# Optimization experiments

Measured on AMD Instinct MI355X. Metric: run time of the kernel, lower is better.

Reference implementation:

```python
import jax, jax.numpy as jnp
import numpy as np

EPS = 1e-4

def _mp_normalize(x):
    # EDM2-style normalize: divide by (eps + RMS-scaled L2 norm) along last dim -> unit RMS
    n = jnp.linalg.norm(x, axis=-1, keepdims=True)
    n = EPS + n * (1.0 / np.sqrt(x.shape[-1]))
    return x / n

def _mp_linear(x, w):
    # magnitude-preserving linear: row-normalized weight scaled by 1/sqrt(fan_in), no bias
    fan_in = w.shape[-1]
    w_hat = _mp_normalize(w) * (1.0 / np.sqrt(fan_in))
    return x @ w_hat.T

def setup_inputs() -> dict:
    key = jax.random.key(0)
    k1, k2, k3 = jax.random.split(key, 3)
    B, T, D = 2, 2048, 1024
    x = jax.random.normal(k1, (B, T, D), dtype=jnp.float32)
    w_qkv = jax.random.normal(k2, (3 * D, D), dtype=jnp.float32)
    w_out = jax.random.normal(k3, (D, D), dtype=jnp.float32)
    return {"x": x, "w_qkv": w_qkv, "w_out": w_out}

def reference(x, w_qkv, w_out):
    B, T, D = x.shape
    H = 16
    hd = D // H
    scale = 1.0 / np.sqrt(hd)

    qkv = _mp_linear(x, w_qkv)                      # (B, T, 3D)
    q, k, v = jnp.split(qkv, 3, axis=-1)            # each (B, T, D)

    def to_heads(t):
        return t.reshape(B, T, H, hd).transpose(0, 2, 1, 3)  # (B, H, T, hd)

    q, k, v = to_heads(q), to_heads(k), to_heads(v)
    q = _mp_normalize(q)
    k = _mp_normalize(k)

    scores = jnp.einsum("bhqd,bhkd->bhqk", q, k) * scale
    attn = jax.nn.softmax(scores, axis=-1)
    out = jnp.einsum("bhqk,bhkd->bhqd", attn, v)    # (B, H, T, hd)
    out = out.transpose(0, 2, 1, 3).reshape(B, T, D)
    return _mp_linear(out, w_out)
```

## Files before the change

kernel.cpp:

```cpp
#include <hip/hip_runtime.h>

#define BATCH  2
#define SEQ    2048
#define DMODEL 1024
#define NHEAD  16
#define HDIM   64
#define NROWS  (BATCH * SEQ)
#define QKVC   (3 * DMODEL)

typedef float f32x4 __attribute__((ext_vector_type(4)));
typedef float f32x16 __attribute__((ext_vector_type(16)));
typedef short s16x8 __attribute__((ext_vector_type(8)));
typedef short s16x4 __attribute__((ext_vector_type(4)));
typedef unsigned int u32x4 __attribute__((ext_vector_type(4)));

__device__ __forceinline__ unsigned short f2bf(float f) {
  unsigned int u = __float_as_uint(f);
  u = (u + 0x7FFFu + ((u >> 16) & 1u)) >> 16;
  return (unsigned short)u;
}
__device__ __forceinline__ float bf2f(unsigned short s) {
  return __uint_as_float(((unsigned int)s) << 16);
}
__device__ __forceinline__ unsigned pkbf(float a, float b) {
  unsigned r;
  asm("v_cvt_pk_bf16_f32 %0, %1, %2" : "=v"(r) : "v"(a), "v"(b));
  return r;
}
__device__ __forceinline__ void swp(unsigned &a, unsigned &b) {
  asm volatile("v_permlane32_swap_b32 %0, %1" : "+v"(a), "+v"(b));
}

__global__ __launch_bounds__(256) void k_wnorm(const float* __restrict__ Wq_src,
                                               const float* __restrict__ Wo_src,
                                               unsigned short* __restrict__ Wq,
                                               unsigned short* __restrict__ Wo) {
  const int row = blockIdx.x, tid = threadIdx.x;
  const float* src = (row < QKVC) ? (Wq_src + (size_t)row * DMODEL)
                                  : (Wo_src + (size_t)(row - QKVC) * DMODEL);
  unsigned short* dst = (row < QKVC) ? (Wq + (size_t)row * DMODEL)
                                     : (Wo + (size_t)(row - QKVC) * DMODEL);
  float4 v = ((const float4*)src)[tid];
  float ss = v.x * v.x + v.y * v.y + v.z * v.z + v.w * v.w;
#pragma unroll
  for (int m = 1; m < 64; m <<= 1) ss += __shfl_xor(ss, m);
  __shared__ float part[4];
  if ((tid & 63) == 0) part[tid >> 6] = ss;
  __syncthreads();
  const float tot = part[0] + part[1] + part[2] + part[3];
  const float scale = 0.03125f / (1e-4f + sqrtf(tot) * 0.03125f);
  unsigned short* op = dst + tid * 4;
  op[0] = f2bf(v.x * scale); op[1] = f2bf(v.y * scale);
  op[2] = f2bf(v.z * scale); op[3] = f2bf(v.w * scale);
}

__global__ __launch_bounds__(256) void k_cast(const float* __restrict__ X,
                                              unsigned short* __restrict__ Xb) {
  const int i = blockIdx.x * 256 + threadIdx.x;
  const float4 v = ((const float4*)X)[i];
  ushort4 o = { f2bf(v.x), f2bf(v.y), f2bf(v.z), f2bf(v.w) };
  ((ushort4*)Xb)[i] = o;
}

#define LDP 88
template <int WRITE_BF16>
__global__ __launch_bounds__(256, 3) void k_gemm_bt(const unsigned short* __restrict__ A,
                                                    const unsigned short* __restrict__ Bm,
                                                    void* __restrict__ Cv,
                                                    int M, int N, int K) {
  __shared__ unsigned short As[128 * LDP];
  __shared__ unsigned short Bs[128 * LDP];
  const int tid = threadIdx.x;
  const int nbn = N >> 7;
  const int bm = (blockIdx.x / nbn) << 7;
  const int bn = (blockIdx.x % nbn) << 7;
  const int wave = tid >> 6, lane = tid & 63;
  const int wr = (wave >> 1) << 6, wc = (wave & 1) << 6;
  const int l16 = lane & 15, lg = lane >> 4;

  f32x4 acc[4][4];
#pragma unroll
  for (int m = 0; m < 4; ++m)
#pragma unroll
    for (int n = 0; n < 4; ++n) acc[m][n] = (f32x4){0.f, 0.f, 0.f, 0.f};

  s16x8 ra[4], rb[4];
#pragma unroll
  for (int it = 0; it < 4; ++it) {
    const int c = it * 256 + tid;
    const int r = c >> 3, col = (c & 7) << 3;
    ra[it] = *(const s16x8*)(A + (size_t)(bm + r) * K + col);
    rb[it] = *(const s16x8*)(Bm + (size_t)(bn + r) * K + col);
  }

  for (int k0 = 0; k0 < K; k0 += 64) {
    __syncthreads();
#pragma unroll
    for (int it = 0; it < 4; ++it) {
      const int c = it * 256 + tid;
      const int r = c >> 3, col = (c & 7) << 3;
      *(s16x8*)(As + r * LDP + col) = ra[it];
      *(s16x8*)(Bs + r * LDP + col) = rb[it];
    }
    __syncthreads();
    if (k0 + 64 < K) {
#pragma unroll
      for (int it = 0; it < 4; ++it) {
        const int c = it * 256 + tid;
        const int r = c >> 3, col = (c & 7) << 3;
        ra[it] = *(const s16x8*)(A + (size_t)(bm + r) * K + k0 + 64 + col);
        rb[it] = *(const s16x8*)(Bm + (size_t)(bn + r) * K + k0 + 64 + col);
      }
    }
#pragma unroll
    for (int ks = 0; ks < 2; ++ks) {
      s16x8 af[4], bq[4];
#pragma unroll
      for (int m = 0; m < 4; ++m)
        af[m] = *(const s16x8*)(As + (wr + m * 16 + l16) * LDP + ks * 32 + lg * 8);
#pragma unroll
      for (int n = 0; n < 4; ++n)
        bq[n] = *(const s16x8*)(Bs + (wc + n * 16 + l16) * LDP + ks * 32 + lg * 8);
#pragma unroll
      for (int m = 0; m < 4; ++m)
#pragma unroll
        for (int n = 0; n < 4; ++n)
          acc[m][n] = __builtin_amdgcn_mfma_f32_16x16x32_bf16(af[m], bq[n], acc[m][n], 0, 0, 0);
    }
  }
  if (WRITE_BF16) {
    unsigned short* C = (unsigned short*)Cv;
#pragma unroll
    for (int m = 0; m < 4; ++m)
#pragma unroll
      for (int n = 0; n < 4; ++n)
#pragma unroll
        for (int r = 0; r < 4; ++r)
          C[(size_t)(bm + wr + m * 16 + lg * 4 + r) * N + (bn + wc + n * 16 + l16)] =
              f2bf(acc[m][n][r]);
  } else {
    float* C = (float*)Cv;
#pragma unroll
    for (int m = 0; m < 4; ++m)
#pragma unroll
      for (int n = 0; n < 4; ++n)
#pragma unroll
        for (int r = 0; r < 4; ++r)
          C[(size_t)(bm + wr + m * 16 + lg * 4 + r) * N + (bn + wc + n * 16 + l16)] =
              acc[m][n][r];
  }
}

__global__ __launch_bounds__(256) void k_qknorm(unsigned short* __restrict__ qkv) {
  const int row = blockIdx.x, tid = threadIdx.x;
  const int hv = tid >> 3, g = tid & 7;
  const int base = (hv < 16) ? (hv * HDIM) : (DMODEL + (hv - 16) * HDIM);
  unsigned short* p = qkv + (size_t)row * QKVC + base + g * 8;
  s16x8 v = *(const s16x8*)p;
  float f[8];
  float ss = 0.f;
#pragma unroll
  for (int j = 0; j < 8; ++j) { f[j] = bf2f((unsigned short)v[j]); ss += f[j] * f[j]; }
  ss += __shfl_xor(ss, 1); ss += __shfl_xor(ss, 2); ss += __shfl_xor(ss, 4);
  float scale = 1.f / (1e-4f + sqrtf(ss) * 0.125f);
  if (hv < 16) scale *= 0.125f;
  s16x8 o;
#pragma unroll
  for (int j = 0; j < 8; ++j) o[j] = (short)f2bf(f[j] * scale);
  *(s16x8*)p = o;
}

__global__ __launch_bounds__(256) void k_vtrans(const unsigned short* __restrict__ qkv,
                                                unsigned short* __restrict__ Vt) {
  const int tt = blockIdx.x & 31, bh = blockIdx.x >> 5;
  const int b = bh >> 4, h = bh & 15;
  const int t0 = tt * 64;
  __shared__ unsigned short tile[64][80];
  const int tid = threadIdx.x;
#pragma unroll
  for (int half = 0; half < 2; ++half) {
    const int tl = half * 32 + (tid >> 3), part = tid & 7;
    s16x8 v = *(const s16x8*)(qkv + (size_t)(b * SEQ + t0 + tl) * QKVC + 2 * DMODEL +
                              h * HDIM + part * 8);
    *(s16x8*)(&tile[tl][part * 8]) = v;
  }
  __syncthreads();
#pragma unroll
  for (int half = 0; half < 2; ++half) {
    const int d = half * 32 + (tid >> 3), tp = tid & 7;
    s16x8 o;
#pragma unroll
    for (int j = 0; j < 8; ++j) o[j] = (short)tile[tp * 8 + j][d];
    *(s16x8*)(Vt + (size_t)(bh * HDIM + d) * SEQ + t0 + tp * 8) = o;
  }
}

__global__ __launch_bounds__(256) void k_attn(const unsigned short* __restrict__ qkv,
                                              const unsigned short* __restrict__ Vt,
                                              unsigned short* __restrict__ O) {
  const int bid = blockIdx.x;
  const int logical = ((bid & 7) << 6) + (bid >> 3);
  const int bh = logical >> 4, qt = logical & 15;
  const int b = bh >> 4, h = bh & 15;
  const int tid = threadIdx.x;
  const int wave = tid >> 6, lane = tid & 63;
  const int l31 = lane & 31, hi = lane >> 5;
  const int q0 = qt * 128 + wave * 32;

  __shared__ s16x8 ks[64 * 8];
  __shared__ s16x8 vs[64 * 8];

  const unsigned short* qp =
      qkv + (size_t)(b * SEQ + q0 + l31) * QKVC + h * HDIM + hi * 8;
  const s16x8 qf0 = *(const s16x8*)(qp);
  const s16x8 qf1 = *(const s16x8*)(qp + 16);
  const s16x8 qf2 = *(const s16x8*)(qp + 32);
  const s16x8 qf3 = *(const s16x8*)(qp + 48);

  const int srow = tid >> 3, chunk = tid & 7;
  const unsigned short* ksrc =
      qkv + (size_t)(b * SEQ + srow) * QKVC + DMODEL + h * HDIM + chunk * 8;
  const unsigned short* vsrc =
      Vt + (size_t)(bh * HDIM + srow) * SEQ + chunk * 8;
  const int wsl = srow * 8 + (chunk ^ (srow & 7));
  const int wsh = wsl + 32 * 8;

  f32x16 acc0 = {0,0,0,0,0,0,0,0,0,0,0,0,0,0,0,0};
  f32x16 acc1 = {0,0,0,0,0,0,0,0,0,0,0,0,0,0,0,0};
  float l = 0.f;

  s16x8 rk0 = *(const s16x8*)(ksrc);
  s16x8 rk1 = *(const s16x8*)(ksrc + (size_t)32 * QKVC);
  s16x8 rv0 = *(const s16x8*)(vsrc);
  s16x8 rv1 = *(const s16x8*)(vsrc + (size_t)32 * SEQ);

  for (int kt = 0; kt < SEQ; kt += 64) {
    __syncthreads();
    ks[wsl] = rk0; ks[wsh] = rk1;
    vs[wsl] = rv0; vs[wsh] = rv1;
    __syncthreads();
    if (kt + 64 < SEQ) {
      rk0 = *(const s16x8*)(ksrc + (size_t)(kt + 64) * QKVC);
      rk1 = *(const s16x8*)(ksrc + (size_t)(kt + 96) * QKVC);
      rv0 = *(const s16x8*)(vsrc + kt + 64);
      rv1 = *(const s16x8*)(vsrc + (size_t)32 * SEQ + kt + 64);
    }
#pragma unroll
    for (int kh = 0; kh < 2; ++kh) {
      const int key = kh * 32 + l31;
      const int kb = key * 8, kx = key & 7;
      f32x16 st = {0,0,0,0,0,0,0,0,0,0,0,0,0,0,0,0};
      st = __builtin_amdgcn_mfma_f32_32x32x16_bf16(ks[kb + ((0 + hi) ^ kx)], qf0, st, 0, 0, 0);
      st = __builtin_amdgcn_mfma_f32_32x32x16_bf16(ks[kb + ((2 + hi) ^ kx)], qf1, st, 0, 0, 0);
      st = __builtin_amdgcn_mfma_f32_32x32x16_bf16(ks[kb + ((4 + hi) ^ kx)], qf2, st, 0, 0, 0);
      st = __builtin_amdgcn_mfma_f32_32x32x16_bf16(ks[kb + ((6 + hi) ^ kx)], qf3, st, 0, 0, 0);

#pragma unroll
      for (int r = 0; r < 16; ++r) st[r] = __expf(st[r] - 8.f);

      float s0 = (st[0] + st[1]) + (st[2] + st[3]);
      float s1 = (st[4] + st[5]) + (st[6] + st[7]);
      float s2 = (st[8] + st[9]) + (st[10] + st[11]);
      float s3 = (st[12] + st[13]) + (st[14] + st[15]);
      l += (s0 + s1) + (s2 + s3);

      unsigned P0 = pkbf(st[0], st[1]),   P1 = pkbf(st[2], st[3]);
      unsigned P2 = pkbf(st[4], st[5]),   P3 = pkbf(st[6], st[7]);
      unsigned P4 = pkbf(st[8], st[9]),   P5 = pkbf(st[10], st[11]);
      unsigned P6 = pkbf(st[12], st[13]), P7 = pkbf(st[14], st[15]);
      swp(P0, P2);
      swp(P1, P3);
      swp(P4, P6);
      swp(P5, P7);
      u32x4 w0; w0[0] = P0; w0[1] = P1; w0[2] = P2; w0[3] = P3;
      u32x4 w1; w1[0] = P4; w1[1] = P5; w1[2] = P6; w1[3] = P7;
      const s16x8 pf0 = __builtin_bit_cast(s16x8, w0);
      const s16x8 pf1 = __builtin_bit_cast(s16x8, w1);

      const int vb0 = l31 * 8,        vx0 = l31 & 7;
      const int vb1 = (l31 + 32) * 8, vx1 = vx0;
      acc0 = __builtin_amdgcn_mfma_f32_32x32x16_bf16(vs[vb0 + ((kh * 4 + 0 + hi) ^ vx0)], pf0, acc0, 0, 0, 0);
      acc0 = __builtin_amdgcn_mfma_f32_32x32x16_bf16(vs[vb0 + ((kh * 4 + 2 + hi) ^ vx0)], pf1, acc0, 0, 0, 0);
      acc1 = __builtin_amdgcn_mfma_f32_32x32x16_bf16(vs[vb1 + ((kh * 4 + 0 + hi) ^ vx1)], pf0, acc1, 0, 0, 0);
      acc1 = __builtin_amdgcn_mfma_f32_32x32x16_bf16(vs[vb1 + ((kh * 4 + 2 + hi) ^ vx1)], pf1, acc1, 0, 0, 0);
    }
  }

  l += __shfl_xor(l, 32);

  const float inv = 1.f / l;
  unsigned short* ob = O + (size_t)(b * SEQ + q0 + l31) * DMODEL + h * HDIM;
#pragma unroll
  for (int g = 0; g < 4; ++g) {
    s16x4 o0 = { (short)f2bf(acc0[4 * g] * inv),     (short)f2bf(acc0[4 * g + 1] * inv),
                 (short)f2bf(acc0[4 * g + 2] * inv), (short)f2bf(acc0[4 * g + 3] * inv) };
    s16x4 o1 = { (short)f2bf(acc1[4 * g] * inv),     (short)f2bf(acc1[4 * g + 1] * inv),
                 (short)f2bf(acc1[4 * g + 2] * inv), (short)f2bf(acc1[4 * g + 3] * inv) };
    *(s16x4*)(ob + g * 8 + hi * 4) = o0;
    *(s16x4*)(ob + 32 + g * 8 + hi * 4) = o1;
  }
}

extern "C" void kernel_launch(void* const* d_in, const int* in_sizes, int n_in,
                              void* d_out, int out_size, void* d_ws, size_t ws_size,
                              hipStream_t stream) {
  const float* x    = (const float*)d_in[0];
  const float* wqkv = (const float*)d_in[1];
  const float* wout = (const float*)d_in[2];
  char* ws = (char*)d_ws;
  unsigned short* Wq  = (unsigned short*)(ws);
  unsigned short* Wo  = (unsigned short*)(ws + 6291456);
  unsigned short* Xb  = (unsigned short*)(ws + 8388608);
  unsigned short* QKV = (unsigned short*)(ws + 16777216);
  unsigned short* Vt  = (unsigned short*)(ws + 41943040);
  (void)in_sizes; (void)n_in; (void)out_size; (void)ws_size;

  k_wnorm<<<QKVC + DMODEL, 256, 0, stream>>>(wqkv, wout, Wq, Wo);
  k_cast<<<(NROWS * DMODEL) / 1024, 256, 0, stream>>>(x, Xb);
  k_gemm_bt<1><<<(NROWS / 128) * (QKVC / 128), 256, 0, stream>>>(
      Xb, Wq, (void*)QKV, NROWS, QKVC, DMODEL);
  k_qknorm<<<NROWS, 256, 0, stream>>>(QKV);
  k_vtrans<<<BATCH * NHEAD * (SEQ / 64), 256, 0, stream>>>(QKV, Vt);
  k_attn<<<BATCH * NHEAD * 16, 256, 0, stream>>>(QKV, Vt, Xb);
  k_gemm_bt<0><<<(NROWS / 128) * (DMODEL / 128), 256, 0, stream>>>(
      Xb, Wo, d_out, NROWS, DMODEL, DMODEL);
}
```

Baseline: 133.2 us.

## Split attention keys across two wave groups and merge partial outputs via LDS

The attention kernel now launches 512 threads per block. Two groups of four waves each handle half of the key sequence for the same 128 queries. The partial accumulators and row sums are combined through shared memory at the end. This doubles the waves available to hide MFMA and exp latency, since only 512 blocks exist across the GPU. In exchange the register prefetch of the next K/V tile is dropped, so loads are now issued just before the barrier and exposed. The change also adds LDS traffic and an extra synchronization for the reduction.

```diff
diff --git a/kernel.cpp b/kernel.cpp
--- a/kernel.cpp
+++ b/kernel.cpp
@@ -195,7 +195,7 @@
   }
 }
 
-__global__ __launch_bounds__(256) void k_attn(const unsigned short* __restrict__ qkv,
+__global__ __launch_bounds__(512) void k_attn(const unsigned short* __restrict__ qkv,
                                               const unsigned short* __restrict__ Vt,
                                               unsigned short* __restrict__ O) {
   const int bid = blockIdx.x;
@@ -205,10 +205,14 @@
   const int tid = threadIdx.x;
   const int wave = tid >> 6, lane = tid & 63;
   const int l31 = lane & 31, hi = lane >> 5;
-  const int q0 = qt * 128 + wave * 32;
-
-  __shared__ s16x8 ks[64 * 8];
-  __shared__ s16x8 vs[64 * 8];
+  const int qw = wave & 3, half = wave >> 2;
+  const int q0 = qt * 128 + qw * 32;
+
+  __shared__ s16x8 smem[2048];
+  __shared__ float LL[4][64];
+
+  s16x8* ksh = smem + half * 512;
+  s16x8* vsh = smem + 1024 + half * 512;
 
   const unsigned short* qp =
       qkv + (size_t)(b * SEQ + q0 + l31) * QKVC + h * HDIM + hi * 8;
@@ -217,43 +221,37 @@
   const s16x8 qf2 = *(const s16x8*)(qp + 32);
   const s16x8 qf3 = *(const s16x8*)(qp + 48);
 
-  const int srow = tid >> 3, chunk = tid & 7;
+  const int t8 = tid & 255;
+  const int srow = t8 >> 3, chunk = t8 & 7;
   const unsigned short* ksrc =
-      qkv + (size_t)(b * SEQ + srow) * QKVC + DMODEL + h * HDIM + chunk * 8;
+      qkv + (size_t)(b * SEQ + half * 1024 + srow) * QKVC + DMODEL + h * HDIM + chunk * 8;
   const unsigned short* vsrc =
-      Vt + (size_t)(bh * HDIM + srow) * SEQ + chunk * 8;
+      Vt + (size_t)(bh * HDIM + srow) * SEQ + half * 1024 + chunk * 8;
   const int wsl = srow * 8 + (chunk ^ (srow & 7));
-  const int wsh = wsl + 32 * 8;
+  const int wsh = wsl + 256;
 
   f32x16 acc0 = {0,0,0,0,0,0,0,0,0,0,0,0,0,0,0,0};
   f32x16 acc1 = {0,0,0,0,0,0,0,0,0,0,0,0,0,0,0,0};
   float l = 0.f;
 
-  s16x8 rk0 = *(const s16x8*)(ksrc);
-  s16x8 rk1 = *(const s16x8*)(ksrc + (size_t)32 * QKVC);
-  s16x8 rv0 = *(const s16x8*)(vsrc);
-  s16x8 rv1 = *(const s16x8*)(vsrc + (size_t)32 * SEQ);
-
-  for (int kt = 0; kt < SEQ; kt += 64) {
+  for (int kt = 0; kt < 1024; kt += 64) {
+    const s16x8 rk0 = *(const s16x8*)(ksrc + (size_t)kt * QKVC);
+    const s16x8 rk1 = *(const s16x8*)(ksrc + (size_t)(kt + 32) * QKVC);
+    const s16x8 rv0 = *(const s16x8*)(vsrc + kt);
+    const s16x8 rv1 = *(const s16x8*)(vsrc + (size_t)32 * SEQ + kt);
     __syncthreads();
-    ks[wsl] = rk0; ks[wsh] = rk1;
-    vs[wsl] = rv0; vs[wsh] = rv1;
+    ksh[wsl] = rk0; ksh[wsh] = rk1;
+    vsh[wsl] = rv0; vsh[wsh] = rv1;
     __syncthreads();
-    if (kt + 64 < SEQ) {
-      rk0 = *(const s16x8*)(ksrc + (size_t)(kt + 64) * QKVC);
-      rk1 = *(const s16x8*)(ksrc + (size_t)(kt + 96) * QKVC);
-      rv0 = *(const s16x8*)(vsrc + kt + 64);
-      rv1 = *(const s16x8*)(vsrc + (size_t)32 * SEQ + kt + 64);
-    }
 #pragma unroll
     for (int kh = 0; kh < 2; ++kh) {
       const int key = kh * 32 + l31;
       const int kb = key * 8, kx = key & 7;
       f32x16 st = {0,0,0,0,0,0,0,0,0,0,0,0,0,0,0,0};
-      st = __builtin_amdgcn_mfma_f32_32x32x16_bf16(ks[kb + ((0 + hi) ^ kx)], qf0, st, 0, 0, 0);
-      st = __builtin_amdgcn_mfma_f32_32x32x16_bf16(ks[kb + ((2 + hi) ^ kx)], qf1, st, 0, 0, 0);
-      st = __builtin_amdgcn_mfma_f32_32x32x16_bf16(ks[kb + ((4 + hi) ^ kx)], qf2, st, 0, 0, 0);
-      st = __builtin_amdgcn_mfma_f32_32x32x16_bf16(ks[kb + ((6 + hi) ^ kx)], qf3, st, 0, 0, 0);
+      st = __builtin_amdgcn_mfma_f32_32x32x16_bf16(ksh[kb + ((0 + hi) ^ kx)], qf0, st, 0, 0, 0);
+      st = __builtin_amdgcn_mfma_f32_32x32x16_bf16(ksh[kb + ((2 + hi) ^ kx)], qf1, st, 0, 0, 0);
+      st = __builtin_amdgcn_mfma_f32_32x32x16_bf16(ksh[kb + ((4 + hi) ^ kx)], qf2, st, 0, 0, 0);
+      st = __builtin_amdgcn_mfma_f32_32x32x16_bf16(ksh[kb + ((6 + hi) ^ kx)], qf3, st, 0, 0, 0);
 
 #pragma unroll
       for (int r = 0; r < 16; ++r) st[r] = __expf(st[r] - 8.f);
@@ -279,25 +277,46 @@
 
       const int vb0 = l31 * 8,        vx0 = l31 & 7;
       const int vb1 = (l31 + 32) * 8, vx1 = vx0;
-      acc0 = __builtin_amdgcn_mfma_f32_32x32x16_bf16(vs[vb0 + ((kh * 4 + 0 + hi) ^ vx0)], pf0, acc0, 0, 0, 0);
-      acc0 = __builtin_amdgcn_mfma_f32_32x32x16_bf16(vs[vb0 + ((kh * 4 + 2 + hi) ^ vx0)], pf1, acc0, 0, 0, 0);
-      acc1 = __builtin_amdgcn_mfma_f32_32x32x16_bf16(vs[vb1 + ((kh * 4 + 0 + hi) ^ vx1)], pf0, acc1, 0, 0, 0);
-      acc1 = __builtin_amdgcn_mfma_f32_32x32x16_bf16(vs[vb1 + ((kh * 4 + 2 + hi) ^ vx1)], pf1, acc1, 0, 0, 0);
+      acc0 = __builtin_amdgcn_mfma_f32_32x32x16_bf16(vsh[vb0 + ((kh * 4 + 0 + hi) ^ vx0)], pf0, acc0, 0, 0, 0);
+      acc0 = __builtin_amdgcn_mfma_f32_32x32x16_bf16(vsh[vb0 + ((kh * 4 + 2 + hi) ^ vx0)], pf1, acc0, 0, 0, 0);
+      acc1 = __builtin_amdgcn_mfma_f32_32x32x16_bf16(vsh[vb1 + ((kh * 4 + 0 + hi) ^ vx1)], pf0, acc1, 0, 0, 0);
+      acc1 = __builtin_amdgcn_mfma_f32_32x32x16_bf16(vsh[vb1 + ((kh * 4 + 2 + hi) ^ vx1)], pf1, acc1, 0, 0, 0);
     }
   }
 
   l += __shfl_xor(l, 32);
 
-  const float inv = 1.f / l;
-  unsigned short* ob = O + (size_t)(b * SEQ + q0 + l31) * DMODEL + h * HDIM;
-#pragma unroll
-  for (int g = 0; g < 4; ++g) {
-    s16x4 o0 = { (short)f2bf(acc0[4 * g] * inv),     (short)f2bf(acc0[4 * g + 1] * inv),
-                 (short)f2bf(acc0[4 * g + 2] * inv), (short)f2bf(acc0[4 * g + 3] * inv) };
-    s16x4 o1 = { (short)f2bf(acc1[4 * g] * inv),     (short)f2bf(acc1[4 * g + 1] * inv),
-                 (short)f2bf(acc1[4 * g + 2] * inv), (short)f2bf(acc1[4 * g + 3] * inv) };
-    *(s16x4*)(ob + g * 8 + hi * 4) = o0;
-    *(s16x4*)(ob + 32 + g * 8 + hi * 4) = o1;
+  __syncthreads();
+  float* OO = (float*)smem;
+  if (half) {
+    float* o_ = OO + qw * 2048;
+#pragma unroll
+    for (int r = 0; r < 16; ++r) {
+      o_[r * 64 + lane] = acc0[r];
+      o_[(16 + r) * 64 + lane] = acc1[r];
+    }
+    LL[qw][lane] = l;
+  }
+  __syncthreads();
+  if (!half) {
+    const float inv = 1.f / (l + LL[qw][lane]);
+    const float* o_ = OO + qw * 2048;
+    unsigned short* ob = O + (size_t)(b * SEQ + q0 + l31) * DMODEL + h * HDIM;
+#pragma unroll
+    for (int g = 0; g < 4; ++g) {
+      float e00 = (acc0[4 * g]     + o_[(4 * g) * 64 + lane])     * inv;
+      float e01 = (acc0[4 * g + 1] + o_[(4 * g + 1) * 64 + lane]) * inv;
+      float e02 = (acc0[4 * g + 2] + o_[(4 * g + 2) * 64 + lane]) * inv;
+      float e03 = (acc0[4 * g + 3] + o_[(4 * g + 3) * 64 + lane]) * inv;
+      float e10 = (acc1[4 * g]     + o_[(16 + 4 * g) * 64 + lane])     * inv;
+      float e11 = (acc1[4 * g + 1] + o_[(16 + 4 * g + 1) * 64 + lane]) * inv;
+      float e12 = (acc1[4 * g + 2] + o_[(16 + 4 * g + 2) * 64 + lane]) * inv;
+      float e13 = (acc1[4 * g + 3] + o_[(16 + 4 * g + 3) * 64 + lane]) * inv;
+      s16x4 o0 = { (short)f2bf(e00), (short)f2bf(e01), (short)f2bf(e02), (short)f2bf(e03) };
+      s16x4 o1 = { (short)f2bf(e10), (short)f2bf(e11), (short)f2bf(e12), (short)f2bf(e13) };
+      *(s16x4*)(ob + g * 8 + hi * 4) = o0;
+      *(s16x4*)(ob + 32 + g * 8 + hi * 4) = o1;
+    }
   }
 }
 
@@ -321,7 +340,7 @@
       Xb, Wq, (void*)QKV, NROWS, QKVC, DMODEL);
   k_qknorm<<<NROWS, 256, 0, stream>>>(QKV);
   k_vtrans<<<BATCH * NHEAD * (SEQ / 64), 256, 0, stream>>>(QKV, Vt);
-  k_attn<<<BATCH * NHEAD * 16, 256, 0, stream>>>(QKV, Vt, Xb);
+  k_attn<<<BATCH * NHEAD * 16, 512, 0, stream>>>(QKV, Vt, Xb);
   k_gemm_bt<0><<<(NROWS / 128) * (DMODEL / 128), 256, 0, stream>>>(
       Xb, Wo, d_out, NROWS, DMODEL, DMODEL);
 }
```

Result: faster. 122.7 us (-7.9%).
